# Kernel tuning notes

Hardware: AMD Instinct MI355X
Metric: run time of the kernel (lower is better)

## Reference

```python
import jax, jax.numpy as jnp
import numpy as np

WS = 11      # window_size
SIGMA = 1.5
C = 3        # channels
C1 = 0.01 ** 2
C2 = 0.03 ** 2


def _gauss_window(ws=WS, sigma=SIGMA, channel=C):
    x = np.arange(ws, dtype=np.float64) - ws // 2
    g = np.exp(-(x ** 2) / (2.0 * sigma ** 2))
    g = g / g.sum()
    w2 = np.outer(g, g).astype(np.float32)            # [ws, ws]
    w = np.broadcast_to(w2, (channel, 1, ws, ws)).copy()  # depthwise OIHW
    return jnp.asarray(w)


def _dwconv(x, w):
    # depthwise conv2d, SAME padding (kernel 11 odd -> pad 5, matches torch)
    return jax.lax.conv_general_dilated(
        x, w, window_strides=(1, 1), padding='SAME',
        feature_group_count=w.shape[0],
        dimension_numbers=('NCHW', 'OIHW', 'NCHW'))


def setup_inputs() -> dict:
    key = jax.random.key(0)
    k1, k2 = jax.random.split(key)
    img1 = jax.random.uniform(k1, (16, 3, 512, 512), dtype=jnp.float32)
    img2 = jax.random.uniform(k2, (16, 3, 512, 512), dtype=jnp.float32)
    window = _gauss_window()
    return {'img1': img1, 'img2': img2, 'window': window}


def reference(img1, img2, window):
    # forward clamps to [0,1] when out of range; uniform inputs are in-range,
    # so clip is a faithful no-op here.
    img1 = jnp.clip(img1, 0.0, 1.0)
    img2 = jnp.clip(img2, 0.0, 1.0)

    mu1 = _dwconv(img1, window)
    mu2 = _dwconv(img2, window)
    mu1_sq = mu1 * mu1
    mu2_sq = mu2 * mu2
    mu1_mu2 = mu1 * mu2

    sigma1_sq = _dwconv(img1 * img1, window) - mu1_sq
    sigma2_sq = _dwconv(img2 * img2, window) - mu2_sq
    sigma12 = _dwconv(img1 * img2, window) - mu1_mu2

    ssim_map = ((2.0 * mu1_mu2 + C1) * (2.0 * sigma12 + C2)) / (
        (mu1_sq + mu2_sq + C1) * (sigma1_sq + sigma2_sq + C2))
    ssim_map = jnp.clip(ssim_map, 0.0, 1.0)

    ssim_value = jnp.mean(ssim_map)            # size_average=True
    return jnp.maximum(1.0 - ssim_value, 0.0)  # clamp(loss, min=0)
```

## Files before the change

### kernel.cpp

```cpp
#include <hip/hip_runtime.h>
#include <math.h>

typedef short bf16x8 __attribute__((ext_vector_type(8)));
typedef float f32x4 __attribute__((ext_vector_type(4)));
typedef float f32x2 __attribute__((ext_vector_type(2)));
typedef unsigned short u16;

#define NT 256
#define TSTR 50
#define C1c 1e-4f
#define C2c 9e-4f

__device__ inline u16 f2bf(float f) {
    unsigned u = __float_as_uint(f);
    return (u16)((u + 0x7FFFu + ((u >> 16) & 1u)) >> 16);
}
__device__ inline float bf2f(u16 h) { return __uint_as_float((unsigned)h << 16); }

template <bool ATOMIC>
__global__ __launch_bounds__(NT) void ssim_mfma3(
    const float* __restrict__ img1, const float* __restrict__ img2,
    const float* __restrict__ window, float* __restrict__ partials)
{
    __shared__ alignas(16) u16 T[5][64 * TSTR];
    __shared__ u16 wtab[64];
    __shared__ float wred[4];

    const int tid = threadIdx.x;
    const int x0 = blockIdx.x * 64;
    const int y0 = blockIdx.y * 32;
    const float* p1 = img1 + (size_t)blockIdx.z * (512 * 512);
    const float* p2 = img2 + (size_t)blockIdx.z * (512 * 512);

    if (tid < 64 && (tid < 20 || tid > 30)) wtab[tid] = 0;
    if (tid == 0) {
        float inv = 1.0f / sqrtf(window[60]);
        float carry = 0.f;
        for (int k = 0; k < 11; ++k) {
            float gk = window[55 + k] * inv + carry;
            u16 q = f2bf(gk);
            carry = gk - bf2f(q);
            wtab[20 + k] = q;
        }
    }
    __syncthreads();

    const int lane = tid & 63;
    const int lrow = lane & 15;
    const int lgrp = lane >> 4;
    const int wid = tid >> 6;

    bf16x8 wB, wA;
    #pragma unroll
    for (int j = 0; j < 8; ++j) {
        int k = lgrp * 8 + j;
        wB[j] = (short)wtab[17 + k - lrow];
        wA[j] = (short)wtab[20 + k - lrow];
    }
    f32x4 z4 = {0.f, 0.f, 0.f, 0.f};

    const bool interior = (x0 >= 8) && (x0 <= 440) && (y0 >= 5) && (y0 <= 469);

    for (int p = wid; p < 12; p += 4) {
        int m1 = p >> 2;
        int n1 = wid;
        int gy = y0 - 5 + 16 * m1 + lrow;
        int gxb = x0 - 8 + 16 * n1 + 8 * lgrp;

        float4 A0 = make_float4(0.f,0.f,0.f,0.f), A1 = A0, B0 = A0, B1 = A0;
        if (interior) {
            const float* r1 = p1 + gy * 512 + gxb;
            const float* r2 = p2 + gy * 512 + gxb;
            A0 = *(const float4*)(r1);
            A1 = *(const float4*)(r1 + 4);
            B0 = *(const float4*)(r2);
            B1 = *(const float4*)(r2 + 4);
        } else {
            bool yok = (unsigned)gy < 512u;
            if (yok && gxb >= 0 && gxb <= 508) {
                A0 = *(const float4*)(p1 + gy * 512 + gxb);
                B0 = *(const float4*)(p2 + gy * 512 + gxb);
            }
            int gxb4 = gxb + 4;
            if (yok && gxb4 >= 0 && gxb4 <= 508) {
                A1 = *(const float4*)(p1 + gy * 512 + gxb4);
                B1 = *(const float4*)(p2 + gy * 512 + gxb4);
            }
        }
        float xa[8] = {A0.x, A0.y, A0.z, A0.w, A1.x, A1.y, A1.z, A1.w};
        float xb[8] = {B0.x, B0.y, B0.z, B0.w, B1.x, B1.y, B1.z, B1.w};

        unsigned ua[4], ub[4], uaa[4], ubb[4], uab[4];
        #pragma unroll
        for (int w = 0; w < 4; ++w) {
            f32x2 va = {xa[2*w], xa[2*w+1]};
            f32x2 vb = {xb[2*w], xb[2*w+1]};
            f32x2 vaa = va * va;
            f32x2 vbb = vb * vb;
            f32x2 vab = va * vb;
            asm("v_cvt_pk_bf16_f32 %0, %1, %2" : "=v"(ua[w])  : "v"(va.x),  "v"(va.y));
            asm("v_cvt_pk_bf16_f32 %0, %1, %2" : "=v"(ub[w])  : "v"(vb.x),  "v"(vb.y));
            asm("v_cvt_pk_bf16_f32 %0, %1, %2" : "=v"(uaa[w]) : "v"(vaa.x), "v"(vaa.y));
            asm("v_cvt_pk_bf16_f32 %0, %1, %2" : "=v"(ubb[w]) : "v"(vbb.x), "v"(vbb.y));
            asm("v_cvt_pk_bf16_f32 %0, %1, %2" : "=v"(uab[w]) : "v"(vab.x), "v"(vab.y));
        }
        bf16x8 fa  = __builtin_bit_cast(bf16x8, make_uint4(ua[0],  ua[1],  ua[2],  ua[3]));
        bf16x8 fb  = __builtin_bit_cast(bf16x8, make_uint4(ub[0],  ub[1],  ub[2],  ub[3]));
        bf16x8 faa = __builtin_bit_cast(bf16x8, make_uint4(uaa[0], uaa[1], uaa[2], uaa[3]));
        bf16x8 fbb = __builtin_bit_cast(bf16x8, make_uint4(ubb[0], ubb[1], ubb[2], ubb[3]));
        bf16x8 fab = __builtin_bit_cast(bf16x8, make_uint4(uab[0], uab[1], uab[2], uab[3]));

        f32x4 c0 = __builtin_amdgcn_mfma_f32_16x16x32_bf16(fa,  wB, z4, 0, 0, 0);
        f32x4 c1 = __builtin_amdgcn_mfma_f32_16x16x32_bf16(fb,  wB, z4, 0, 0, 0);
        f32x4 c2 = __builtin_amdgcn_mfma_f32_16x16x32_bf16(faa, wB, z4, 0, 0, 0);
        f32x4 c3 = __builtin_amdgcn_mfma_f32_16x16x32_bf16(fbb, wB, z4, 0, 0, 0);
        f32x4 c4 = __builtin_amdgcn_mfma_f32_16x16x32_bf16(fab, wB, z4, 0, 0, 0);

        int tx = 16 * n1 + lrow;
        int te = tx * TSTR + 16 * m1 + 4 * lgrp;
        {
            unsigned lo, hi;
            asm("v_cvt_pk_bf16_f32 %0, %1, %2" : "=v"(lo) : "v"(c0[0]), "v"(c0[1]));
            asm("v_cvt_pk_bf16_f32 %0, %1, %2" : "=v"(hi) : "v"(c0[2]), "v"(c0[3]));
            *(uint2*)&T[0][te] = make_uint2(lo, hi);
            asm("v_cvt_pk_bf16_f32 %0, %1, %2" : "=v"(lo) : "v"(c1[0]), "v"(c1[1]));
            asm("v_cvt_pk_bf16_f32 %0, %1, %2" : "=v"(hi) : "v"(c1[2]), "v"(c1[3]));
            *(uint2*)&T[1][te] = make_uint2(lo, hi);
            asm("v_cvt_pk_bf16_f32 %0, %1, %2" : "=v"(lo) : "v"(c2[0]), "v"(c2[1]));
            asm("v_cvt_pk_bf16_f32 %0, %1, %2" : "=v"(hi) : "v"(c2[2]), "v"(c2[3]));
            *(uint2*)&T[2][te] = make_uint2(lo, hi);
            asm("v_cvt_pk_bf16_f32 %0, %1, %2" : "=v"(lo) : "v"(c3[0]), "v"(c3[1]));
            asm("v_cvt_pk_bf16_f32 %0, %1, %2" : "=v"(hi) : "v"(c3[2]), "v"(c3[3]));
            *(uint2*)&T[3][te] = make_uint2(lo, hi);
            asm("v_cvt_pk_bf16_f32 %0, %1, %2" : "=v"(lo) : "v"(c4[0]), "v"(c4[1]));
            asm("v_cvt_pk_bf16_f32 %0, %1, %2" : "=v"(hi) : "v"(c4[2]), "v"(c4[3]));
            *(uint2*)&T[4][te] = make_uint2(lo, hi);
        }
    }
    __syncthreads();

    float lsum = 0.f;
    for (int p = wid; p < 8; p += 4) {
        int m2 = p >> 2;
        int n2 = wid;
        int tx = 16 * n2 + lrow;
        int te = tx * TSTR + 16 * m2 + 8 * lgrp;
        f32x4 cf[5];
        #pragma unroll
        for (int f = 0; f < 5; ++f) {
            uint4 q = *(const uint4*)&T[f][te];
            cf[f] = __builtin_amdgcn_mfma_f32_16x16x32_bf16(wA, __builtin_bit_cast(bf16x8, q), z4, 0, 0, 0);
        }
        #pragma unroll
        for (int pr = 0; pr < 2; ++pr) {
            f32x2 mu1 = {cf[0][2*pr], cf[0][2*pr+1]};
            f32x2 mu2 = {cf[1][2*pr], cf[1][2*pr+1]};
            f32x2 e11 = {cf[2][2*pr], cf[2][2*pr+1]};
            f32x2 e22 = {cf[3][2*pr], cf[3][2*pr+1]};
            f32x2 e12 = {cf[4][2*pr], cf[4][2*pr+1]};
            f32x2 m11 = mu1 * mu1, m22 = mu2 * mu2, m12 = mu1 * mu2;
            f32x2 s1  = e11 - m11;
            f32x2 s2  = e22 - m22;
            f32x2 s12 = e12 - m12;
            f32x2 num = (2.f * m12 + C1c) * (2.f * s12 + C2c);
            f32x2 den = (m11 + m22 + C1c) * (s1 + s2 + C2c);
            float v0 = num.x * __builtin_amdgcn_rcpf(den.x);
            float v1 = num.y * __builtin_amdgcn_rcpf(den.y);
            lsum += fminf(fmaxf(v0, 0.f), 1.f) + fminf(fmaxf(v1, 0.f), 1.f);
        }
    }

    #pragma unroll
    for (int off = 32; off > 0; off >>= 1) lsum += __shfl_down(lsum, off);
    if ((tid & 63) == 0) wred[wid] = lsum;
    __syncthreads();
    if (tid == 0) {
        float bsum = wred[0] + wred[1] + wred[2] + wred[3];
        int bid = (blockIdx.z * gridDim.y + blockIdx.y) * gridDim.x + blockIdx.x;
        if (ATOMIC) atomicAdd(&partials[0], bsum);
        else        partials[bid] = bsum;
    }
}

__global__ void ssim_finalize(const float* __restrict__ partials, int n,
                              float* __restrict__ out, float inv_npx)
{
    __shared__ float w[4];
    float s = 0.f;
    for (int i = threadIdx.x; i < n; i += 256) s += partials[i];
    #pragma unroll
    for (int off = 32; off > 0; off >>= 1) s += __shfl_down(s, off);
    if ((threadIdx.x & 63) == 0) w[threadIdx.x >> 6] = s;
    __syncthreads();
    if (threadIdx.x == 0) {
        float total = w[0] + w[1] + w[2] + w[3];
        float loss = 1.0f - total * inv_npx;
        out[0] = fmaxf(loss, 0.0f);
    }
}

extern "C" void kernel_launch(void* const* d_in, const int* in_sizes, int n_in,
                              void* d_out, int out_size, void* d_ws, size_t ws_size,
                              hipStream_t stream) {
    const float* img1   = (const float*)d_in[0];
    const float* img2   = (const float*)d_in[1];
    const float* window = (const float*)d_in[2];
    float* out      = (float*)d_out;
    float* partials = (float*)d_ws;

    int planes = in_sizes[0] >> 18;
    dim3 grid(512 / 64, 512 / 32, planes);
    int npart = grid.x * grid.y * grid.z;
    float inv_npx = 1.0f / (float)in_sizes[0];

    if (ws_size >= (size_t)npart * sizeof(float)) {
        ssim_mfma3<false><<<grid, NT, 0, stream>>>(img1, img2, window, partials);
        ssim_finalize<<<1, 256, 0, stream>>>(partials, npart, out, inv_npx);
    } else {
        hipMemsetAsync(d_ws, 0, sizeof(float), stream);
        ssim_mfma3<true><<<grid, NT, 0, stream>>>(img1, img2, window, partials);
        ssim_finalize<<<1, 256, 0, stream>>>(partials, 1, out, inv_npx);
    }
}
```

Before: 53.50 us.

## Double output tile height and overlap second-half loads with first-half pass two

```diff
diff --git a/kernel.cpp b/kernel.cpp
--- a/kernel.cpp
+++ b/kernel.cpp
@@ -7,7 +7,7 @@
 typedef unsigned short u16;
 
 #define NT 256
-#define TSTR 50
+#define TSTR 82
 #define C1c 1e-4f
 #define C2c 9e-4f
 
@@ -18,7 +18,7 @@
 __device__ inline float bf2f(u16 h) { return __uint_as_float((unsigned)h << 16); }
 
 template <bool ATOMIC>
-__global__ __launch_bounds__(NT) void ssim_mfma3(
+__global__ __launch_bounds__(NT) void ssim_mfma7(
     const float* __restrict__ img1, const float* __restrict__ img2,
     const float* __restrict__ window, float* __restrict__ partials)
 {
@@ -28,7 +28,7 @@
 
     const int tid = threadIdx.x;
     const int x0 = blockIdx.x * 64;
-    const int y0 = blockIdx.y * 32;
+    const int y0 = blockIdx.y * 64;
     const float* p1 = img1 + (size_t)blockIdx.z * (512 * 512);
     const float* p2 = img2 + (size_t)blockIdx.z * (512 * 512);
 
@@ -59,15 +59,15 @@
     }
     f32x4 z4 = {0.f, 0.f, 0.f, 0.f};
 
-    const bool interior = (x0 >= 8) && (x0 <= 440) && (y0 >= 5) && (y0 <= 469);
-
-    for (int p = wid; p < 12; p += 4) {
-        int m1 = p >> 2;
-        int n1 = wid;
+    const bool interior = (x0 >= 8) && (x0 <= 440) && (y0 >= 5) && (y0 <= 437);
+
+    const int n1 = wid;
+    const int gxb = x0 - 8 + 16 * n1 + 8 * lgrp;
+
+    auto ld = [&](int m1, float4& A0, float4& A1, float4& B0, float4& B1) {
         int gy = y0 - 5 + 16 * m1 + lrow;
-        int gxb = x0 - 8 + 16 * n1 + 8 * lgrp;
-
-        float4 A0 = make_float4(0.f,0.f,0.f,0.f), A1 = A0, B0 = A0, B1 = A0;
+        float4 z = make_float4(0.f, 0.f, 0.f, 0.f);
+        A0 = z; A1 = z; B0 = z; B1 = z;
         if (interior) {
             const float* r1 = p1 + gy * 512 + gxb;
             const float* r2 = p2 + gy * 512 + gxb;
@@ -87,9 +87,11 @@
                 B1 = *(const float4*)(p2 + gy * 512 + gxb4);
             }
         }
+    };
+
+    auto p1c = [&](int m1, float4 A0, float4 A1, float4 B0, float4 B1) {
         float xa[8] = {A0.x, A0.y, A0.z, A0.w, A1.x, A1.y, A1.z, A1.w};
         float xb[8] = {B0.x, B0.y, B0.z, B0.w, B1.x, B1.y, B1.z, B1.w};
-
         unsigned ua[4], ub[4], uaa[4], ubb[4], uab[4];
         #pragma unroll
         for (int w = 0; w < 4; ++w) {
@@ -118,33 +120,28 @@
 
         int tx = 16 * n1 + lrow;
         int te = tx * TSTR + 16 * m1 + 4 * lgrp;
-        {
-            unsigned lo, hi;
-            asm("v_cvt_pk_bf16_f32 %0, %1, %2" : "=v"(lo) : "v"(c0[0]), "v"(c0[1]));
-            asm("v_cvt_pk_bf16_f32 %0, %1, %2" : "=v"(hi) : "v"(c0[2]), "v"(c0[3]));
-            *(uint2*)&T[0][te] = make_uint2(lo, hi);
-            asm("v_cvt_pk_bf16_f32 %0, %1, %2" : "=v"(lo) : "v"(c1[0]), "v"(c1[1]));
-            asm("v_cvt_pk_bf16_f32 %0, %1, %2" : "=v"(hi) : "v"(c1[2]), "v"(c1[3]));
-            *(uint2*)&T[1][te] = make_uint2(lo, hi);
-            asm("v_cvt_pk_bf16_f32 %0, %1, %2" : "=v"(lo) : "v"(c2[0]), "v"(c2[1]));
-            asm("v_cvt_pk_bf16_f32 %0, %1, %2" : "=v"(hi) : "v"(c2[2]), "v"(c2[3]));
-            *(uint2*)&T[2][te] = make_uint2(lo, hi);
-            asm("v_cvt_pk_bf16_f32 %0, %1, %2" : "=v"(lo) : "v"(c3[0]), "v"(c3[1]));
-            asm("v_cvt_pk_bf16_f32 %0, %1, %2" : "=v"(hi) : "v"(c3[2]), "v"(c3[3]));
-            *(uint2*)&T[3][te] = make_uint2(lo, hi);
-            asm("v_cvt_pk_bf16_f32 %0, %1, %2" : "=v"(lo) : "v"(c4[0]), "v"(c4[1]));
-            asm("v_cvt_pk_bf16_f32 %0, %1, %2" : "=v"(hi) : "v"(c4[2]), "v"(c4[3]));
-            *(uint2*)&T[4][te] = make_uint2(lo, hi);
-        }
-    }
-    __syncthreads();
+        unsigned lo, hi;
+        asm("v_cvt_pk_bf16_f32 %0, %1, %2" : "=v"(lo) : "v"(c0[0]), "v"(c0[1]));
+        asm("v_cvt_pk_bf16_f32 %0, %1, %2" : "=v"(hi) : "v"(c0[2]), "v"(c0[3]));
+        *(uint2*)&T[0][te] = make_uint2(lo, hi);
+        asm("v_cvt_pk_bf16_f32 %0, %1, %2" : "=v"(lo) : "v"(c1[0]), "v"(c1[1]));
+        asm("v_cvt_pk_bf16_f32 %0, %1, %2" : "=v"(hi) : "v"(c1[2]), "v"(c1[3]));
+        *(uint2*)&T[1][te] = make_uint2(lo, hi);
+        asm("v_cvt_pk_bf16_f32 %0, %1, %2" : "=v"(lo) : "v"(c2[0]), "v"(c2[1]));
+        asm("v_cvt_pk_bf16_f32 %0, %1, %2" : "=v"(hi) : "v"(c2[2]), "v"(c2[3]));
+        *(uint2*)&T[2][te] = make_uint2(lo, hi);
+        asm("v_cvt_pk_bf16_f32 %0, %1, %2" : "=v"(lo) : "v"(c3[0]), "v"(c3[1]));
+        asm("v_cvt_pk_bf16_f32 %0, %1, %2" : "=v"(hi) : "v"(c3[2]), "v"(c3[3]));
+        *(uint2*)&T[3][te] = make_uint2(lo, hi);
+        asm("v_cvt_pk_bf16_f32 %0, %1, %2" : "=v"(lo) : "v"(c4[0]), "v"(c4[1]));
+        asm("v_cvt_pk_bf16_f32 %0, %1, %2" : "=v"(hi) : "v"(c4[2]), "v"(c4[3]));
+        *(uint2*)&T[4][te] = make_uint2(lo, hi);
+    };
 
     float lsum = 0.f;
-    for (int p = wid; p < 8; p += 4) {
-        int m2 = p >> 2;
-        int n2 = wid;
-        int tx = 16 * n2 + lrow;
-        int te = tx * TSTR + 16 * m2 + 8 * lgrp;
+    auto p2c = [&](int m2) {
+        const int tx = 16 * wid + lrow;
+        const int te = tx * TSTR + 16 * m2 + 8 * lgrp;
         f32x4 cf[5];
         #pragma unroll
         for (int f = 0; f < 5; ++f) {
@@ -168,7 +165,27 @@
             float v1 = num.y * __builtin_amdgcn_rcpf(den.y);
             lsum += fminf(fmaxf(v0, 0.f), 1.f) + fminf(fmaxf(v1, 0.f), 1.f);
         }
-    }
+    };
+
+    {
+        float4 A0, A1, B0, B1;
+        ld(0, A0, A1, B0, B1); p1c(0, A0, A1, B0, B1);
+        ld(1, A0, A1, B0, B1); p1c(1, A0, A1, B0, B1);
+        ld(2, A0, A1, B0, B1); p1c(2, A0, A1, B0, B1);
+    }
+    __syncthreads();
+
+    float4 A30, A31, B30, B31, A40, A41, B40, B41;
+    ld(3, A30, A31, B30, B31);
+    ld(4, A40, A41, B40, B41);
+    p2c(0);
+    p2c(1);
+    p1c(3, A30, A31, B30, B31);
+    p1c(4, A40, A41, B40, B41);
+    __syncthreads();
+
+    p2c(2);
+    p2c(3);
 
     #pragma unroll
     for (int off = 32; off > 0; off >>= 1) lsum += __shfl_down(lsum, off);
@@ -209,16 +226,16 @@
     float* partials = (float*)d_ws;
 
     int planes = in_sizes[0] >> 18;
-    dim3 grid(512 / 64, 512 / 32, planes);
+    dim3 grid(512 / 64, 512 / 64, planes);
     int npart = grid.x * grid.y * grid.z;
     float inv_npx = 1.0f / (float)in_sizes[0];
 
     if (ws_size >= (size_t)npart * sizeof(float)) {
-        ssim_mfma3<false><<<grid, NT, 0, stream>>>(img1, img2, window, partials);
+        ssim_mfma7<false><<<grid, NT, 0, stream>>>(img1, img2, window, partials);
         ssim_finalize<<<1, 256, 0, stream>>>(partials, npart, out, inv_npx);
     } else {
         hipMemsetAsync(d_ws, 0, sizeof(float), stream);
-        ssim_mfma3<true><<<grid, NT, 0, stream>>>(img1, img2, window, partials);
+        ssim_mfma7<true><<<grid, NT, 0, stream>>>(img1, img2, window, partials);
         ssim_finalize<<<1, 256, 0, stream>>>(partials, 1, out, inv_npx);
     }
 }
```

Result: slower. 63.07 us (+17.9%).
